# Kernel tuning notes

Hardware: AMD Instinct MI355X
Metric: run time of the kernel (lower is better)

The kernel has to match this reference:

```python
import jax, jax.numpy as jnp
import numpy as np

B, T, N, F_IN, F_OUT, K = 16, 12, 1024, 32, 64, 3


def _make_cheb(key, n, k):
    # random symmetric 'scaled laplacian' in [-1, 1]-ish, then Chebyshev recurrence
    a = jax.random.normal(key, (n, n), dtype=jnp.float32) * 0.02
    L = (a + a.T) * 0.5
    polys = [jnp.eye(n, dtype=jnp.float32), L]
    for i in range(2, k):
        polys.append(2.0 * L @ polys[-1] - polys[-2])
    return jnp.stack(polys[:k], axis=0)  # [K, N, N]


def setup_inputs() -> dict:
    key = jax.random.key(0)
    k1, k2, k3, k4 = jax.random.split(key, 4)
    x = jax.random.normal(k1, (B, T, N, F_IN), dtype=jnp.float32)
    spatial_attention = jax.random.uniform(k2, (B, N, N), dtype=jnp.float32)
    cheb = _make_cheb(k3, N, K)
    # xavier-uniform-ish init for Theta [K, F_in, F_out]
    limit = float(np.sqrt(6.0 / (F_IN + F_OUT)))
    Theta = jax.random.uniform(k4, (K, F_IN, F_OUT), dtype=jnp.float32,
                               minval=-limit, maxval=limit)
    return {"x": x, "spatial_attention": spatial_attention, "cheb": cheb, "Theta": Theta}


def reference(x, spatial_attention, cheb, Theta):
    # T_k_at[b,k,i,j] = cheb[k,i,j] * att[b,i,j]   (mask-multiply)
    tk_at = cheb[None, :, :, :] * spatial_attention[:, None, :, :]  # [B,K,N,N]
    # rhs[b,t,k,i,f] = sum_j tk_at[b,k,i,j] * x[b,t,j,f]
    rhs = jnp.einsum('bkij,btjf->btkif', tk_at, x)
    # out[b,t,i,o] = sum_{k,f} rhs[b,t,k,i,f] * Theta[k,f,o], then ReLU
    out = jnp.einsum('btkif,kfo->btio', rhs, Theta)
    return jax.nn.relu(out)
```

## Files before the change

kernel.cpp:

```cpp
#include <hip/hip_runtime.h>

#define Bb 16
#define Tt 12
#define Nn 1024
#define FIN 32
#define FOUT 64
#define KC 3
#define TF (Tt * FIN)
#define NO (Tt * FOUT)

#define BM 128
#define BN 192
#define BK 64
#define NKT (Nn / BK)

typedef __attribute__((ext_vector_type(8))) short short8;
typedef __attribute__((ext_vector_type(4))) float f32x4;

__device__ __forceinline__ unsigned short f2bf(float f) {
  union { float f; unsigned u; } v; v.f = f;
  unsigned r = v.u + 0x7FFFu + ((v.u >> 16) & 1u);
  return (unsigned short)(r >> 16);
}

__device__ __forceinline__ void BAR() {
  __builtin_amdgcn_sched_barrier(0);
  __builtin_amdgcn_s_barrier();
  __builtin_amdgcn_sched_barrier(0);
}

__global__ __launch_bounds__(256) void k2r_build_YxT(
    const float* __restrict__ x, unsigned short* __restrict__ YxT) {
  __shared__ float xs[256][33];
  const int tid = threadIdx.x;
  const int bid = blockIdx.x;
  const int jc = bid & 3;
  const int bt = bid >> 2;
  const int t = bt % Tt, b = bt / Tt;
  const int j0 = jc * 256;
  const float* xp = x + ((size_t)(b * Tt + t) * Nn + j0) * FIN;
#pragma unroll
  for (int m = 0; m < 8; ++m) {
    const int flat = m * 256 + tid;
    const int j_loc = flat >> 3, f4 = flat & 7;
    const float4 v = *(const float4*)(xp + (size_t)j_loc * FIN + f4 * 4);
    xs[j_loc][f4 * 4 + 0] = v.x; xs[j_loc][f4 * 4 + 1] = v.y;
    xs[j_loc][f4 * 4 + 2] = v.z; xs[j_loc][f4 * 4 + 3] = v.w;
  }
  __syncthreads();
  const int f = tid >> 3, jg = tid & 7;
  unsigned short* dst = YxT + ((size_t)b * TF + t * FIN + f) * Nn + j0 + jg * 32;
#pragma unroll
  for (int m = 0; m < 4; ++m) {
    short8 sh;
#pragma unroll
    for (int e = 0; e < 8; ++e)
      sh[e] = (short)f2bf(xs[jg * 32 + m * 8 + e][f]);
    *(short8*)(dst + m * 8) = sh;
  }
}

__global__ __launch_bounds__(512, 4) void k3f_gemm(
    const float* __restrict__ att, const float* __restrict__ cheb,
    const unsigned short* __restrict__ YxT, unsigned short* __restrict__ rhs) {
  __shared__ __align__(16) unsigned short lds[40960];
  const int bid = blockIdx.x;
  const int logical = (bid & 7) * 96 + (bid >> 3);
  const int g = logical / 6, m = logical % 6;
  const int b  = g >> 3;
  const int it = g & 7;
  const int kk = m >> 1;
  const int nt = m & 1;
  const int bk = b * 3 + kk;
  const float* Aa = att  + ((size_t)b  * Nn + it * BM) * Nn;
  const float* Ac = cheb + ((size_t)kk * Nn + it * BM) * Nn;
  const unsigned short* Bp = YxT + ((size_t)b * TF + nt * BN) * Nn;
  const int tid = threadIdx.x;
  const int w = tid >> 6, l = tid & 63;
  const int wm = w >> 2, wn = w & 3;
  const int lrow = l & 15;
  const int c0 = l >> 4;
  const int sx = lrow & 7;

  f32x4 acc[4][3];
#pragma unroll
  for (int mi = 0; mi < 4; ++mi)
#pragma unroll
    for (int ni = 0; ni < 3; ++ni)
      acc[mi][ni] = (f32x4){0.f, 0.f, 0.f, 0.f};

  float4 ra[4], rc[4];

  auto ISSUE = [&](int kt) {
#pragma unroll
    for (int u = 0; u < 2; ++u) {
      const int idx = u * 512 + tid;
      const int row = idx >> 3, c = idx & 7;
      const float* ap = Aa + (size_t)row * Nn + kt * BK + c * 8;
      const float* cp = Ac + (size_t)row * Nn + kt * BK + c * 8;
      ra[2 * u]     = *(const float4*)ap;
      ra[2 * u + 1] = *(const float4*)(ap + 4);
      rc[2 * u]     = *(const float4*)cp;
      rc[2 * u + 1] = *(const float4*)(cp + 4);
    }
  };

  auto CVTW = [&](int d) {
#pragma unroll
    for (int u = 0; u < 2; ++u) {
      const int idx = u * 512 + tid;
      const int row = idx >> 3, c = idx & 7;
      short8 o;
      o[0] = (short)f2bf(ra[2 * u].x * rc[2 * u].x);
      o[1] = (short)f2bf(ra[2 * u].y * rc[2 * u].y);
      o[2] = (short)f2bf(ra[2 * u].z * rc[2 * u].z);
      o[3] = (short)f2bf(ra[2 * u].w * rc[2 * u].w);
      o[4] = (short)f2bf(ra[2 * u + 1].x * rc[2 * u + 1].x);
      o[5] = (short)f2bf(ra[2 * u + 1].y * rc[2 * u + 1].y);
      o[6] = (short)f2bf(ra[2 * u + 1].z * rc[2 * u + 1].z);
      o[7] = (short)f2bf(ra[2 * u + 1].w * rc[2 * u + 1].w);
      *(short8*)&lds[d * 8192 + row * 64 + (c ^ (row & 7)) * 8] = o;
    }
  };

  auto BDMA = [&](int d, int kt) {
#pragma unroll
    for (int g2 = 0; g2 < 3; ++g2) {
      const int idx = g2 * 512 + tid;
      const int row = idx >> 3;
      const int csrc = (idx & 7) ^ (row & 7);
      __builtin_amdgcn_global_load_lds(
          (const __attribute__((address_space(1))) void*)(Bp + (size_t)row * Nn + kt * BK + csrc * 8),
          (__attribute__((address_space(3))) void*)(lds + 16384 + d * 12288 + (g2 * 512 + w * 64) * 8),
          16, 0, 0);
    }
  };

  auto LDA = [&](int d, int mi, int ks) -> short8 {
    const int row = wm * 64 + mi * 16 + lrow;
    const int ch  = (c0 | (ks << 2)) ^ sx;
    return *(const short8*)&lds[d * 8192 + row * 64 + ch * 8];
  };
  auto LDB = [&](int d, int ni, int ks) -> short8 {
    const int row = wn * 48 + ni * 16 + lrow;
    const int ch  = (c0 | (ks << 2)) ^ sx;
    return *(const short8*)&lds[16384 + d * 12288 + row * 64 + ch * 8];
  };

  ISSUE(0);
  asm volatile("s_waitcnt vmcnt(0)" ::: "memory");
  CVTW(0);
  ISSUE(1);
  BDMA(0, 0);
  BDMA(1, 1);
  asm volatile("s_waitcnt vmcnt(6)" ::: "memory");
  CVTW(1);
  ISSUE(2);
  asm volatile("s_waitcnt vmcnt(0) lgkmcnt(0)" ::: "memory");
  BAR();

  for (int tau = 0; tau < NKT; ++tau) {
    const int d = tau & 1;
    short8 bf[3];
    __builtin_amdgcn_s_setprio(1);
#pragma unroll
    for (int ni = 0; ni < 3; ++ni) bf[ni] = LDB(d, ni, 0);
#pragma unroll
    for (int mi = 0; mi < 4; ++mi) {
      const short8 af = LDA(d, mi, 0);
#pragma unroll
      for (int ni = 0; ni < 3; ++ni)
        acc[mi][ni] = __builtin_amdgcn_mfma_f32_16x16x32_bf16(af, bf[ni], acc[mi][ni], 0, 0, 0);
    }
#pragma unroll
    for (int ni = 0; ni < 3; ++ni) bf[ni] = LDB(d, ni, 1);
#pragma unroll
    for (int mi = 0; mi < 4; ++mi) {
      const short8 af = LDA(d, mi, 1);
#pragma unroll
      for (int ni = 0; ni < 3; ++ni)
        acc[mi][ni] = __builtin_amdgcn_mfma_f32_16x16x32_bf16(af, bf[ni], acc[mi][ni], 0, 0, 0);
    }
    __builtin_amdgcn_s_setprio(0);
    asm volatile("s_waitcnt vmcnt(0) lgkmcnt(0)" ::: "memory");
    BAR();
    if (tau + 2 < NKT) { CVTW(d); BDMA(d, tau + 2); }
    if (tau + 3 < NKT) ISSUE(tau + 3);
    __builtin_amdgcn_sched_barrier(0);
  }
  asm volatile("s_waitcnt vmcnt(0)" ::: "memory");

  unsigned short* Cw = rhs + ((size_t)bk * Nn + it * BM) * TF + nt * BN;
#pragma unroll
  for (int mi = 0; mi < 4; ++mi) {
#pragma unroll
    for (int ni = 0; ni < 3; ++ni) {
      const int col = wn * 48 + ni * 16 + lrow;
      const int row0 = wm * 64 + mi * 16 + c0 * 4;
      unsigned short* op = Cw + (size_t)row0 * TF + col;
      f32x4 v = acc[mi][ni];
#pragma unroll
      for (int q = 0; q < 4; ++q)
        op[(size_t)q * TF] = f2bf(v[q]);
    }
  }
}

__global__ __launch_bounds__(256) void k4_epilogue(
    const unsigned short* __restrict__ rhs, const float* __restrict__ theta,
    float* __restrict__ out) {
  __shared__ float th[KC * FIN * FOUT];
  const int tid = threadIdx.x;
  for (int s = tid; s < KC * FIN * FOUT; s += 256) th[s] = theta[s];
  __syncthreads();
  const int bid = blockIdx.x;
  const int ic = bid & 3;
  const int bt = bid >> 2;
  const int t = bt % Tt, b = bt / Tt;
  const int w = tid >> 6, l = tid & 63;
  const int lrow = l & 15;
  const int c0 = l >> 4;
  const int i0 = ic * 256 + w * 64;

  short8 bfrag[KC][4];
#pragma unroll
  for (int ks = 0; ks < KC; ++ks)
#pragma unroll
    for (int oi = 0; oi < 4; ++oi) {
      short8 bf;
#pragma unroll
      for (int rr = 0; rr < 8; ++rr)
        bf[rr] = (short)f2bf(th[(ks * FIN + c0 * 8 + rr) * FOUT + oi * 16 + lrow]);
      bfrag[ks][oi] = bf;
    }

  f32x4 acc[4][4];
#pragma unroll
  for (int mi = 0; mi < 4; ++mi)
#pragma unroll
    for (int oi = 0; oi < 4; ++oi)
      acc[mi][oi] = (f32x4){0.f, 0.f, 0.f, 0.f};

#pragma unroll
  for (int ks = 0; ks < KC; ++ks) {
#pragma unroll
    for (int mi = 0; mi < 4; ++mi) {
      const short8 af = *(const short8*)(
          rhs + ((size_t)(b * KC + ks) * Nn + i0 + mi * 16 + lrow) * TF + t * FIN + c0 * 8);
#pragma unroll
      for (int oi = 0; oi < 4; ++oi)
        acc[mi][oi] = __builtin_amdgcn_mfma_f32_16x16x32_bf16(af, bfrag[ks][oi], acc[mi][oi], 0, 0, 0);
    }
  }

#pragma unroll
  for (int mi = 0; mi < 4; ++mi) {
#pragma unroll
    for (int oi = 0; oi < 4; ++oi) {
      const int row = i0 + mi * 16 + c0 * 4;
      float* op = out + ((size_t)(b * Tt + t) * Nn + row) * FOUT + oi * 16 + lrow;
      f32x4 v = acc[mi][oi];
#pragma unroll
      for (int q = 0; q < 4; ++q)
        op[(size_t)q * FOUT] = fmaxf(v[q], 0.f);
    }
  }
}

__global__ __launch_bounds__(128) void k_fallback(
    const float* __restrict__ x, const float* __restrict__ att,
    const float* __restrict__ cheb, const float* __restrict__ theta,
    float* __restrict__ out) {
  const int blk = blockIdx.x;
  const int i = blk & 1023;
  const int bt = blk >> 10;
  const int t = bt % Tt, b = bt / Tt;
  __shared__ float rhs[KC * FIN];
  const int tid = threadIdx.x;
  if (tid < KC * FIN) {
    const int k = tid >> 5, f = tid & 31;
    const float* ar = att + ((size_t)b * Nn + i) * Nn;
    const float* cr = cheb + ((size_t)k * Nn + i) * Nn;
    const float* xr = x + ((size_t)(b * Tt + t) * Nn) * FIN + f;
    float s = 0.f;
    for (int j = 0; j < Nn; ++j) s = fmaf(ar[j] * cr[j], xr[(size_t)j * FIN], s);
    rhs[tid] = s;
  }
  __syncthreads();
  if (tid < FOUT) {
    float a = 0.f;
#pragma unroll
    for (int kf = 0; kf < KC * FIN; ++kf) a = fmaf(rhs[kf], theta[kf * FOUT + tid], a);
    out[((size_t)(b * Tt + t) * Nn + i) * FOUT + tid] = fmaxf(a, 0.f);
  }
}

extern "C" void kernel_launch(void* const* d_in, const int* in_sizes, int n_in,
                              void* d_out, int out_size, void* d_ws, size_t ws_size,
                              hipStream_t stream) {
  const float* x     = (const float*)d_in[0];
  const float* att   = (const float*)d_in[1];
  const float* cheb  = (const float*)d_in[2];
  const float* theta = (const float*)d_in[3];
  float* out = (float*)d_out;

  const size_t needYx = (size_t)Bb * TF * Nn * sizeof(unsigned short);
  const size_t needR  = (size_t)Bb * KC * Nn * TF * sizeof(unsigned short);
  if (ws_size >= needYx + needR) {
    unsigned short* YxT = (unsigned short*)d_ws;
    unsigned short* rhs = (unsigned short*)((char*)d_ws + needYx);
    hipLaunchKernelGGL(k2r_build_YxT, dim3(Bb * Tt * 4), dim3(256), 0, stream,
                       x, YxT);
    hipLaunchKernelGGL(k3f_gemm, dim3(48 * (Nn / BM) * (TF / BN)), dim3(512), 0, stream,
                       att, cheb, YxT, rhs);
    hipLaunchKernelGGL(k4_epilogue, dim3(Bb * Tt * 4), dim3(256), 0, stream,
                       rhs, theta, out);
  } else {
    hipLaunchKernelGGL(k_fallback, dim3(Bb * Tt * Nn), dim3(128), 0, stream,
                       x, att, cheb, theta, out);
  }
}
```

Measured before the change: 103.5 us.

## Double-buffer attention/cheb prefetch registers to deepen global-load pipelining

Replaces the single register set for the fp32 attention and cheb tile loads with two alternating sets. The main loop is unrolled by two, and each tile's loads are issued before the preceding compute phase. The full vmcnt(0) drain is replaced by a partial vmcnt(8) wait, so global-load latency can overlap more MFMA work. The cost is 32 more live VGPRs under a 512-thread, 4-block launch bound, which risks spills or lower occupancy.

```diff
diff --git a/kernel.cpp b/kernel.cpp
--- a/kernel.cpp
+++ b/kernel.cpp
@@ -59,6 +59,38 @@
     *(short8*)(dst + m * 8) = sh;
   }
 }
+
+#define ISSUE_SET(RA, RC, kt) do {                                          \
+  _Pragma("unroll")                                                         \
+  for (int u_ = 0; u_ < 2; ++u_) {                                          \
+    const int idx_ = u_ * 512 + tid;                                        \
+    const int row_ = idx_ >> 3, c_ = idx_ & 7;                              \
+    const float* ap_ = Aa + (size_t)row_ * Nn + (kt) * BK + c_ * 8;         \
+    const float* cp_ = Ac + (size_t)row_ * Nn + (kt) * BK + c_ * 8;         \
+    RA[2 * u_]     = *(const float4*)ap_;                                   \
+    RA[2 * u_ + 1] = *(const float4*)(ap_ + 4);                             \
+    RC[2 * u_]     = *(const float4*)cp_;                                   \
+    RC[2 * u_ + 1] = *(const float4*)(cp_ + 4);                             \
+  }                                                                         \
+} while (0)
+
+#define CVTW_SET(RA, RC, D) do {                                            \
+  _Pragma("unroll")                                                         \
+  for (int u_ = 0; u_ < 2; ++u_) {                                          \
+    const int idx_ = u_ * 512 + tid;                                        \
+    const int row_ = idx_ >> 3, c_ = idx_ & 7;                              \
+    short8 o_;                                                              \
+    o_[0] = (short)f2bf(RA[2 * u_].x * RC[2 * u_].x);                       \
+    o_[1] = (short)f2bf(RA[2 * u_].y * RC[2 * u_].y);                       \
+    o_[2] = (short)f2bf(RA[2 * u_].z * RC[2 * u_].z);                       \
+    o_[3] = (short)f2bf(RA[2 * u_].w * RC[2 * u_].w);                       \
+    o_[4] = (short)f2bf(RA[2 * u_ + 1].x * RC[2 * u_ + 1].x);               \
+    o_[5] = (short)f2bf(RA[2 * u_ + 1].y * RC[2 * u_ + 1].y);               \
+    o_[6] = (short)f2bf(RA[2 * u_ + 1].z * RC[2 * u_ + 1].z);               \
+    o_[7] = (short)f2bf(RA[2 * u_ + 1].w * RC[2 * u_ + 1].w);               \
+    *(short8*)&lds[(D) * 8192 + row_ * 64 + (c_ ^ (row_ & 7)) * 8] = o_;    \
+  }                                                                         \
+} while (0)
 
 __global__ __launch_bounds__(512, 4) void k3f_gemm(
     const float* __restrict__ att, const float* __restrict__ cheb,
@@ -89,39 +121,7 @@
     for (int ni = 0; ni < 3; ++ni)
       acc[mi][ni] = (f32x4){0.f, 0.f, 0.f, 0.f};
 
-  float4 ra[4], rc[4];
-
-  auto ISSUE = [&](int kt) {
-#pragma unroll
-    for (int u = 0; u < 2; ++u) {
-      const int idx = u * 512 + tid;
-      const int row = idx >> 3, c = idx & 7;
-      const float* ap = Aa + (size_t)row * Nn + kt * BK + c * 8;
-      const float* cp = Ac + (size_t)row * Nn + kt * BK + c * 8;
-      ra[2 * u]     = *(const float4*)ap;
-      ra[2 * u + 1] = *(const float4*)(ap + 4);
-      rc[2 * u]     = *(const float4*)cp;
-      rc[2 * u + 1] = *(const float4*)(cp + 4);
-    }
-  };
-
-  auto CVTW = [&](int d) {
-#pragma unroll
-    for (int u = 0; u < 2; ++u) {
-      const int idx = u * 512 + tid;
-      const int row = idx >> 3, c = idx & 7;
-      short8 o;
-      o[0] = (short)f2bf(ra[2 * u].x * rc[2 * u].x);
-      o[1] = (short)f2bf(ra[2 * u].y * rc[2 * u].y);
-      o[2] = (short)f2bf(ra[2 * u].z * rc[2 * u].z);
-      o[3] = (short)f2bf(ra[2 * u].w * rc[2 * u].w);
-      o[4] = (short)f2bf(ra[2 * u + 1].x * rc[2 * u + 1].x);
-      o[5] = (short)f2bf(ra[2 * u + 1].y * rc[2 * u + 1].y);
-      o[6] = (short)f2bf(ra[2 * u + 1].z * rc[2 * u + 1].z);
-      o[7] = (short)f2bf(ra[2 * u + 1].w * rc[2 * u + 1].w);
-      *(short8*)&lds[d * 8192 + row * 64 + (c ^ (row & 7)) * 8] = o;
-    }
-  };
+  float4 ra0[4], rc0[4], ra1[4], rc1[4];
 
   auto BDMA = [&](int d, int kt) {
 #pragma unroll
@@ -147,45 +147,58 @@
     return *(const short8*)&lds[16384 + d * 12288 + row * 64 + ch * 8];
   };
 
-  ISSUE(0);
+  auto COMPUTE = [&](int d) {
+    short8 bf[3];
+    __builtin_amdgcn_s_setprio(1);
+#pragma unroll
+    for (int ni = 0; ni < 3; ++ni) bf[ni] = LDB(d, ni, 0);
+#pragma unroll
+    for (int mi = 0; mi < 4; ++mi) {
+      const short8 af = LDA(d, mi, 0);
+#pragma unroll
+      for (int ni = 0; ni < 3; ++ni)
+        acc[mi][ni] = __builtin_amdgcn_mfma_f32_16x16x32_bf16(af, bf[ni], acc[mi][ni], 0, 0, 0);
+    }
+#pragma unroll
+    for (int ni = 0; ni < 3; ++ni) bf[ni] = LDB(d, ni, 1);
+#pragma unroll
+    for (int mi = 0; mi < 4; ++mi) {
+      const short8 af = LDA(d, mi, 1);
+#pragma unroll
+      for (int ni = 0; ni < 3; ++ni)
+        acc[mi][ni] = __builtin_amdgcn_mfma_f32_16x16x32_bf16(af, bf[ni], acc[mi][ni], 0, 0, 0);
+    }
+    __builtin_amdgcn_s_setprio(0);
+  };
+
+  ISSUE_SET(ra0, rc0, 0);
   asm volatile("s_waitcnt vmcnt(0)" ::: "memory");
-  CVTW(0);
-  ISSUE(1);
+  CVTW_SET(ra0, rc0, 0);
+  ISSUE_SET(ra1, rc1, 1);
+  asm volatile("s_waitcnt vmcnt(0)" ::: "memory");
+  CVTW_SET(ra1, rc1, 1);
   BDMA(0, 0);
   BDMA(1, 1);
-  asm volatile("s_waitcnt vmcnt(6)" ::: "memory");
-  CVTW(1);
-  ISSUE(2);
-  asm volatile("s_waitcnt vmcnt(0) lgkmcnt(0)" ::: "memory");
+  ISSUE_SET(ra0, rc0, 2);
+  asm volatile("s_waitcnt vmcnt(8) lgkmcnt(0)" ::: "memory");
   BAR();
 
-  for (int tau = 0; tau < NKT; ++tau) {
-    const int d = tau & 1;
-    short8 bf[3];
-    __builtin_amdgcn_s_setprio(1);
-#pragma unroll
-    for (int ni = 0; ni < 3; ++ni) bf[ni] = LDB(d, ni, 0);
-#pragma unroll
-    for (int mi = 0; mi < 4; ++mi) {
-      const short8 af = LDA(d, mi, 0);
-#pragma unroll
-      for (int ni = 0; ni < 3; ++ni)
-        acc[mi][ni] = __builtin_amdgcn_mfma_f32_16x16x32_bf16(af, bf[ni], acc[mi][ni], 0, 0, 0);
-    }
-#pragma unroll
-    for (int ni = 0; ni < 3; ++ni) bf[ni] = LDB(d, ni, 1);
-#pragma unroll
-    for (int mi = 0; mi < 4; ++mi) {
-      const short8 af = LDA(d, mi, 1);
-#pragma unroll
-      for (int ni = 0; ni < 3; ++ni)
-        acc[mi][ni] = __builtin_amdgcn_mfma_f32_16x16x32_bf16(af, bf[ni], acc[mi][ni], 0, 0, 0);
-    }
-    __builtin_amdgcn_s_setprio(0);
-    asm volatile("s_waitcnt vmcnt(0) lgkmcnt(0)" ::: "memory");
+  for (int tp = 0; tp < NKT / 2; ++tp) {
+    const int t0 = 2 * tp;
+    if (t0 + 3 < NKT) { ISSUE_SET(ra1, rc1, t0 + 3); }
+    COMPUTE(0);
+    if (t0 + 3 < NKT) asm volatile("s_waitcnt vmcnt(8) lgkmcnt(0)" ::: "memory");
+    else              asm volatile("s_waitcnt vmcnt(0) lgkmcnt(0)" ::: "memory");
     BAR();
-    if (tau + 2 < NKT) { CVTW(d); BDMA(d, tau + 2); }
-    if (tau + 3 < NKT) ISSUE(tau + 3);
+    if (t0 + 2 < NKT) { CVTW_SET(ra0, rc0, 0); BDMA(0, t0 + 2); }
+    __builtin_amdgcn_sched_barrier(0);
+    const int t1 = t0 + 1;
+    if (t1 + 3 < NKT) { ISSUE_SET(ra0, rc0, t1 + 3); }
+    COMPUTE(1);
+    if (t1 + 3 < NKT) asm volatile("s_waitcnt vmcnt(8) lgkmcnt(0)" ::: "memory");
+    else              asm volatile("s_waitcnt vmcnt(0) lgkmcnt(0)" ::: "memory");
+    BAR();
+    if (t1 + 2 < NKT) { CVTW_SET(ra1, rc1, 1); BDMA(1, t1 + 2); }
     __builtin_amdgcn_sched_barrier(0);
   }
   asm volatile("s_waitcnt vmcnt(0)" ::: "memory");
```

Measured after the change: 311.9 us. 201% more time.

## Loop all three Chebyshev orders inside one GEMM block to reuse B tiles

Applied to the files above, without the earlier changes.

The GEMM kernel now has each block iterate over all K=3 Chebyshev orders in sequence (48 k-steps) instead of launching separate blocks per order. Per-order results are written out and the accumulators reset at each order boundary. The B-operand (YxT) LDS ring grows from 2 to 4 stages, with partial vmcnt waits so loads run further ahead. This cuts the grid to a third (256 blocks) and the occupancy hint to 2 blocks per CU, which trades parallelism and latency hiding for a deeper prefetch pipeline. The same YxT tile is still reloaded once per order, so L2 traffic for it is unchanged.

```diff
diff --git a/kernel.cpp b/kernel.cpp
--- a/kernel.cpp
+++ b/kernel.cpp
@@ -12,7 +12,8 @@
 #define BM 128
 #define BN 192
 #define BK 64
-#define NKT (Nn / BK)
+#define NKT 16
+#define NIT (KC * NKT)
 
 typedef __attribute__((ext_vector_type(8))) short short8;
 typedef __attribute__((ext_vector_type(4))) float f32x4;
@@ -60,20 +61,17 @@
   }
 }
 
-__global__ __launch_bounds__(512, 4) void k3f_gemm(
+__global__ __launch_bounds__(512, 2) void k3f2_gemm(
     const float* __restrict__ att, const float* __restrict__ cheb,
     const unsigned short* __restrict__ YxT, unsigned short* __restrict__ rhs) {
-  __shared__ __align__(16) unsigned short lds[40960];
+  __shared__ __align__(16) unsigned short lds[65536];
   const int bid = blockIdx.x;
-  const int logical = (bid & 7) * 96 + (bid >> 3);
-  const int g = logical / 6, m = logical % 6;
+  const int logical = (bid & 7) * 32 + (bid >> 3);
+  const int g  = logical >> 1;
   const int b  = g >> 3;
   const int it = g & 7;
-  const int kk = m >> 1;
-  const int nt = m & 1;
-  const int bk = b * 3 + kk;
-  const float* Aa = att  + ((size_t)b  * Nn + it * BM) * Nn;
-  const float* Ac = cheb + ((size_t)kk * Nn + it * BM) * Nn;
+  const int nt = logical & 1;
+  const float* Aa = att + ((size_t)b * Nn + it * BM) * Nn;
   const unsigned short* Bp = YxT + ((size_t)b * TF + nt * BN) * Nn;
   const int tid = threadIdx.x;
   const int w = tid >> 6, l = tid & 63;
@@ -91,13 +89,15 @@
 
   float4 ra[4], rc[4];
 
-  auto ISSUE = [&](int kt) {
+  auto ISSUE = [&](int tt) {
+    const int kkp = tt >> 4, ktp = tt & 15;
+    const float* Ac = cheb + ((size_t)kkp * Nn + it * BM) * Nn;
 #pragma unroll
     for (int u = 0; u < 2; ++u) {
       const int idx = u * 512 + tid;
       const int row = idx >> 3, c = idx & 7;
-      const float* ap = Aa + (size_t)row * Nn + kt * BK + c * 8;
-      const float* cp = Ac + (size_t)row * Nn + kt * BK + c * 8;
+      const float* ap = Aa + (size_t)row * Nn + ktp * BK + c * 8;
+      const float* cp = Ac + (size_t)row * Nn + ktp * BK + c * 8;
       ra[2 * u]     = *(const float4*)ap;
       ra[2 * u + 1] = *(const float4*)(ap + 4);
       rc[2 * u]     = *(const float4*)cp;
@@ -123,15 +123,16 @@
     }
   };
 
-  auto BDMA = [&](int d, int kt) {
+  auto BDMA = [&](int q, int tt) {
+    const int ktp = tt & 15;
 #pragma unroll
     for (int g2 = 0; g2 < 3; ++g2) {
       const int idx = g2 * 512 + tid;
       const int row = idx >> 3;
       const int csrc = (idx & 7) ^ (row & 7);
       __builtin_amdgcn_global_load_lds(
-          (const __attribute__((address_space(1))) void*)(Bp + (size_t)row * Nn + kt * BK + csrc * 8),
-          (__attribute__((address_space(3))) void*)(lds + 16384 + d * 12288 + (g2 * 512 + w * 64) * 8),
+          (const __attribute__((address_space(1))) void*)(Bp + (size_t)row * Nn + ktp * BK + csrc * 8),
+          (__attribute__((address_space(3))) void*)(lds + 16384 + q * 12288 + (g2 * 512 + w * 64) * 8),
           16, 0, 0);
     }
   };
@@ -141,30 +142,29 @@
     const int ch  = (c0 | (ks << 2)) ^ sx;
     return *(const short8*)&lds[d * 8192 + row * 64 + ch * 8];
   };
-  auto LDB = [&](int d, int ni, int ks) -> short8 {
+  auto LDB = [&](int q, int ni, int ks) -> short8 {
     const int row = wn * 48 + ni * 16 + lrow;
     const int ch  = (c0 | (ks << 2)) ^ sx;
-    return *(const short8*)&lds[16384 + d * 12288 + row * 64 + ch * 8];
+    return *(const short8*)&lds[16384 + q * 12288 + row * 64 + ch * 8];
   };
 
   ISSUE(0);
   asm volatile("s_waitcnt vmcnt(0)" ::: "memory");
   CVTW(0);
   ISSUE(1);
-  BDMA(0, 0);
-  BDMA(1, 1);
-  asm volatile("s_waitcnt vmcnt(6)" ::: "memory");
+  asm volatile("s_waitcnt vmcnt(0)" ::: "memory");
   CVTW(1);
+  BDMA(0, 0); BDMA(1, 1); BDMA(2, 2); BDMA(3, 3);
   ISSUE(2);
-  asm volatile("s_waitcnt vmcnt(0) lgkmcnt(0)" ::: "memory");
+  asm volatile("s_waitcnt vmcnt(8) lgkmcnt(0)" ::: "memory");
   BAR();
 
-  for (int tau = 0; tau < NKT; ++tau) {
-    const int d = tau & 1;
+  for (int ii = 0; ii < NIT; ++ii) {
+    const int d = ii & 1, q = ii & 3;
     short8 bf[3];
     __builtin_amdgcn_s_setprio(1);
 #pragma unroll
-    for (int ni = 0; ni < 3; ++ni) bf[ni] = LDB(d, ni, 0);
+    for (int ni = 0; ni < 3; ++ni) bf[ni] = LDB(q, ni, 0);
 #pragma unroll
     for (int mi = 0; mi < 4; ++mi) {
       const short8 af = LDA(d, mi, 0);
@@ -173,7 +173,7 @@
         acc[mi][ni] = __builtin_amdgcn_mfma_f32_16x16x32_bf16(af, bf[ni], acc[mi][ni], 0, 0, 0);
     }
 #pragma unroll
-    for (int ni = 0; ni < 3; ++ni) bf[ni] = LDB(d, ni, 1);
+    for (int ni = 0; ni < 3; ++ni) bf[ni] = LDB(q, ni, 1);
 #pragma unroll
     for (int mi = 0; mi < 4; ++mi) {
       const short8 af = LDA(d, mi, 1);
@@ -182,27 +182,31 @@
         acc[mi][ni] = __builtin_amdgcn_mfma_f32_16x16x32_bf16(af, bf[ni], acc[mi][ni], 0, 0, 0);
     }
     __builtin_amdgcn_s_setprio(0);
-    asm volatile("s_waitcnt vmcnt(0) lgkmcnt(0)" ::: "memory");
+    if (ii <= NIT - 4) asm volatile("s_waitcnt vmcnt(3) lgkmcnt(0)" ::: "memory");
+    else               asm volatile("s_waitcnt vmcnt(0) lgkmcnt(0)" ::: "memory");
     BAR();
-    if (tau + 2 < NKT) { CVTW(d); BDMA(d, tau + 2); }
-    if (tau + 3 < NKT) ISSUE(tau + 3);
+    if ((ii & 15) == 15) {
+      const int kk = ii >> 4;
+      unsigned short* Cw = rhs + ((size_t)(b * KC + kk) * Nn + it * BM) * TF + nt * BN;
+#pragma unroll
+      for (int mi = 0; mi < 4; ++mi) {
+#pragma unroll
+        for (int ni = 0; ni < 3; ++ni) {
+          const int col = wn * 48 + ni * 16 + lrow;
+          const int row0 = wm * 64 + mi * 16 + c0 * 4;
+          unsigned short* op = Cw + (size_t)row0 * TF + col;
+          f32x4 v = acc[mi][ni];
+#pragma unroll
+          for (int qq = 0; qq < 4; ++qq)
+            op[(size_t)qq * TF] = f2bf(v[qq]);
+          acc[mi][ni] = (f32x4){0.f, 0.f, 0.f, 0.f};
+        }
+      }
+    }
+    if (ii + 2 < NIT) CVTW(d);
+    if (ii + 3 < NIT) ISSUE(ii + 3);
+    if (ii + 4 < NIT) BDMA(q, ii + 4);
     __builtin_amdgcn_sched_barrier(0);
-  }
-  asm volatile("s_waitcnt vmcnt(0)" ::: "memory");
-
-  unsigned short* Cw = rhs + ((size_t)bk * Nn + it * BM) * TF + nt * BN;
-#pragma unroll
-  for (int mi = 0; mi < 4; ++mi) {
-#pragma unroll
-    for (int ni = 0; ni < 3; ++ni) {
-      const int col = wn * 48 + ni * 16 + lrow;
-      const int row0 = wm * 64 + mi * 16 + c0 * 4;
-      unsigned short* op = Cw + (size_t)row0 * TF + col;
-      f32x4 v = acc[mi][ni];
-#pragma unroll
-      for (int q = 0; q < 4; ++q)
-        op[(size_t)q * TF] = f2bf(v[q]);
-    }
   }
 }
 
@@ -311,7 +315,7 @@
     unsigned short* rhs = (unsigned short*)((char*)d_ws + needYx);
     hipLaunchKernelGGL(k2r_build_YxT, dim3(Bb * Tt * 4), dim3(256), 0, stream,
                        x, YxT);
-    hipLaunchKernelGGL(k3f_gemm, dim3(48 * (Nn / BM) * (TF / BN)), dim3(512), 0, stream,
+    hipLaunchKernelGGL(k3f2_gemm, dim3(Bb * (Nn / BM) * (TF / BN)), dim3(512), 0, stream,
                        att, cheb, YxT, rhs);
     hipLaunchKernelGGL(k4_epilogue, dim3(Bb * Tt * 4), dim3(256), 0, stream,
                        rhs, theta, out);
```

After: 121.7 us. +17.6%, slower.
